# Optimization experiments

Hardware: AMD Instinct MI355X
Metric: run time of the kernel (lower is better)

The kernel has to match this reference:

```python
import jax, jax.numpy as jnp
import numpy as np

N_NODES = 50000
N_EDGES = 800000
IN_F = 128
OUT_F = 64
ORDER = 3


def _spmm(edge_index, edge_attr, x):
    # out[row] += edge_attr[e] * x[col]  (COO sparse @ dense)
    row, col = edge_index[0], edge_index[1]
    msgs = x[col] * edge_attr[:, None]          # [E, F] gather + scale
    return jax.ops.segment_sum(msgs, row, num_segments=N_NODES)  # scatter-add


def setup_inputs() -> dict:
    key = jax.random.key(0)
    k1, k2, k3, k4 = jax.random.split(key, 4)
    x = jax.random.normal(k1, (N_NODES, IN_F), dtype=jnp.float32)
    edge_index = jax.random.randint(k2, (2, N_EDGES), 0, N_NODES, dtype=jnp.int64)
    edge_attr = jax.random.uniform(k3, (N_EDGES,), dtype=jnp.float32)
    W = jax.random.normal(k4, (OUT_F, IN_F), dtype=jnp.float32) * (1.0 / np.sqrt(IN_F))
    b = jnp.zeros((OUT_F,), dtype=jnp.float32)
    return {"x": x, "edge_index": edge_index, "edge_attr": edge_attr, "W": W, "b": b}


def reference(x, edge_index, edge_attr, W, b):
    # output = Linear(x); then `order` rounds of spmm aggregation
    out = jnp.einsum("ni,oi->no", x, W) + b      # [N, OUT_F]
    for _ in range(ORDER):
        out = _spmm(edge_index, edge_attr, out)
    return out
```

## Files before the change

kernel.cpp:

```cpp
#include <hip/hip_runtime.h>

#define IN_F   128
#define OUT_F  64
#define GR     64
#define EPB    2048
#define HB     64
#define SB     2048

typedef float  f32x4  __attribute__((ext_vector_type(4)));
typedef unsigned int u32x2 __attribute__((ext_vector_type(2)));
typedef short  s16x8  __attribute__((ext_vector_type(8)));

__device__ __forceinline__ unsigned short f2bf(float f) {
    unsigned int u = __float_as_uint(f);
    u += 0x7fffu + ((u >> 16) & 1u);
    return (unsigned short)(u >> 16);
}
__device__ __forceinline__ float bf2f(unsigned short h) {
    return __uint_as_float(((unsigned int)h) << 16);
}

__global__ __launch_bounds__(256) void gemm_hist_mfma_kernel(
    const float* __restrict__ x, const float* __restrict__ W,
    const float* __restrict__ b, unsigned short* __restrict__ outv, int N,
    const int* __restrict__ rowi, int* __restrict__ bparts, int E,
    int gemm_blocks, int hist_blocks) {

    __shared__ unsigned short xls[64][136];
    __shared__ unsigned short wls[64][136];

    const int t = threadIdx.x;

    if ((int)blockIdx.x >= gemm_blocks) {
        __shared__ int hcnt[256];
        hcnt[t] = 0;
        __syncthreads();
        int hb = blockIdx.x - gemm_blocks;
        for (int e = hb * 256 + t; e < E; e += hist_blocks * 256)
            atomicAdd(&hcnt[rowi[e] >> 8], 1);
        __syncthreads();
        bparts[hb * 256 + t] = hcnt[t];
        return;
    }

    const int row0 = blockIdx.x * GR;

    for (int i = t; i < GR * (IN_F / 4); i += 256) {
        int r = i >> 5, c = i & 31;
        int gr = row0 + r;
        float4 v = make_float4(0.f, 0.f, 0.f, 0.f);
        if (gr < N) v = ((const float4*)x)[(size_t)gr * (IN_F / 4) + c];
        ushort4 u = { f2bf(v.x), f2bf(v.y), f2bf(v.z), f2bf(v.w) };
        *(ushort4*)&xls[r][4 * c] = u;
    }
    for (int i = t; i < OUT_F * (IN_F / 4); i += 256) {
        int n = i >> 5, c = i & 31;
        float4 v = ((const float4*)W)[(size_t)n * (IN_F / 4) + c];
        ushort4 u = { f2bf(v.x), f2bf(v.y), f2bf(v.z), f2bf(v.w) };
        *(ushort4*)&wls[n][4 * c] = u;
    }
    __syncthreads();

    const int w  = t >> 6;
    const int l  = t & 63;
    const int lr = l & 15;
    const int lg = l >> 4;

    f32x4 acc[4] = {};
    #pragma unroll
    for (int s = 0; s < 4; ++s) {
        s16x8 af = *(const s16x8*)&xls[w * 16 + lr][s * 32 + lg * 8];
        #pragma unroll
        for (int c = 0; c < 4; ++c) {
            s16x8 bf = *(const s16x8*)&wls[c * 16 + lr][s * 32 + lg * 8];
            acc[c] = __builtin_amdgcn_mfma_f32_16x16x32_bf16(af, bf, acc[c], 0, 0, 0);
        }
    }
    __syncthreads();

    #pragma unroll
    for (int c = 0; c < 4; ++c) {
        float bv = b[c * 16 + lr];
        #pragma unroll
        for (int r = 0; r < 4; ++r) {
            int rowl = w * 16 + lg * 4 + r;
            xls[rowl][c * 16 + lr] = f2bf(acc[c][r] + bv);
        }
    }
    __syncthreads();
    for (int i = t; i < GR * (OUT_F / 4); i += 256) {
        int r = i >> 4, c4 = i & 15;
        int gr = row0 + r;
        if (gr < N) {
            ushort4 u = *(ushort4*)&xls[r][c4 * 4];
            *(ushort4*)&outv[(size_t)gr * OUT_F + c4 * 4] = u;
        }
    }
}

__global__ __launch_bounds__(256) void bscan_kernel(const int* __restrict__ bparts,
                                                    int* __restrict__ bbase,
                                                    int* __restrict__ bcursor,
                                                    int* __restrict__ rowptr,
                                                    int nb, int N, int E) {
    int t = threadIdx.x;
    int a0 = 0, a1 = 0, a2 = 0, a3 = 0;
    if (t < nb) {
        #pragma unroll
        for (int hb = 0; hb < HB; hb += 4) {
            a0 += bparts[(hb + 0) * 256 + t];
            a1 += bparts[(hb + 1) * 256 + t];
            a2 += bparts[(hb + 2) * 256 + t];
            a3 += bparts[(hb + 3) * 256 + t];
        }
    }
    int v = (a0 + a1) + (a2 + a3);
    int lane = t & 63, w = t >> 6;
    int sum = v;
    #pragma unroll
    for (int off = 1; off < 64; off <<= 1) {
        int x = __shfl_up(sum, off, 64);
        if (lane >= off) sum += x;
    }
    __shared__ int wsum[4];
    if (lane == 63) wsum[w] = sum;
    __syncthreads();
    int woff = 0;
    for (int i = 0; i < w; ++i) woff += wsum[i];
    int excl = sum + woff - v;
    if (t <= nb) bbase[t] = excl;
    if (t < nb)  bcursor[t] = excl;
    if (t == 0)  rowptr[N] = E;
}

__global__ __launch_bounds__(512) void bin_kernel(
    const int* __restrict__ rowi, const int* __restrict__ coli,
    const float* __restrict__ attr, int* __restrict__ bcursor,
    unsigned long long* __restrict__ tmp, int E) {
    __shared__ int cnt[256];
    __shared__ int cur[256];
    __shared__ int gbase[256];
    int t = threadIdx.x;
    int e0 = blockIdx.x * EPB;
    if (t < 256) { cnt[t] = 0; cur[t] = 0; }
    __syncthreads();
    int myrow[4];
    #pragma unroll
    for (int i = 0; i < 4; ++i) {
        int e = e0 + i * 512 + t;
        myrow[i] = (e < E) ? rowi[e] : -1;
        if (myrow[i] >= 0) atomicAdd(&cnt[myrow[i] >> 8], 1);
    }
    __syncthreads();
    if (t < 256 && cnt[t] > 0) gbase[t] = atomicAdd(&bcursor[t], cnt[t]);
    __syncthreads();
    #pragma unroll
    for (int i = 0; i < 4; ++i) {
        int e = e0 + i * 512 + t;
        if (myrow[i] >= 0) {
            int b = myrow[i] >> 8;
            int rank = atomicAdd(&cur[b], 1);
            unsigned long long rec = ((unsigned long long)(myrow[i] & 255) << 32)
                                   | ((unsigned int)coli[e] << 16)
                                   | (unsigned int)f2bf(attr[e]);
            tmp[(size_t)gbase[b] + rank] = rec;
        }
    }
}

__global__ __launch_bounds__(1024) void bsort_kernel(
    const unsigned long long* __restrict__ tmp, const int* __restrict__ bbase,
    unsigned int* __restrict__ scv, int* __restrict__ rowptr, int N) {
    __shared__ int cnt[256];
    __shared__ int cur[256];
    __shared__ int wsum[4];
    int t = threadIdx.x, b = blockIdx.x;
    int seg = bbase[b], segend = bbase[b + 1];
    if (t < 256) cnt[t] = 0;
    __syncthreads();
    for (int i = seg + t; i < segend; i += 1024)
        atomicAdd(&cnt[(int)(tmp[i] >> 32)], 1);
    __syncthreads();
    int v = (t < 256) ? cnt[t] : 0;
    int lane = t & 63, w = t >> 6;
    int sum = v;
    #pragma unroll
    for (int off = 1; off < 64; off <<= 1) {
        int x = __shfl_up(sum, off, 64);
        if (lane >= off) sum += x;
    }
    if (lane == 63 && w < 4) wsum[w] = sum;
    __syncthreads();
    if (t < 256) {
        int woff = 0;
        for (int i = 0; i < w; ++i) woff += wsum[i];
        int excl = sum + woff - v;
        int gidx = b * 256 + t;
        if (gidx <= N) rowptr[gidx] = seg + excl;
        cur[t] = excl;
    }
    __syncthreads();
    for (int i = seg + t; i < segend; i += 1024) {
        unsigned long long rec = tmp[i];
        int rl = (int)(rec >> 32);
        int pos = atomicAdd(&cur[rl], 1);
        scv[(size_t)seg + pos] = (unsigned int)rec;
    }
}

#define FMA4(w, p)                                              \
    a0 = fmaf((w), __uint_as_float((p).x << 16), a0);           \
    a1 = fmaf((w), __uint_as_float((p).x & 0xffff0000u), a1);   \
    a2 = fmaf((w), __uint_as_float((p).y << 16), a2);           \
    a3 = fmaf((w), __uint_as_float((p).y & 0xffff0000u), a3)

template <bool BF16OUT>
__global__ __launch_bounds__(256) void spmm_csr_kernel(
    const int* __restrict__ rowptr, const unsigned int* __restrict__ scv,
    const unsigned short* __restrict__ in, void* __restrict__ outv,
    int N, int nwaves) {
    int gw = (blockIdx.x * 256 + threadIdx.x) >> 6;
    int lane = threadIdx.x & 63;
    int rpw = (N + nwaves - 1) / nwaves;
    int r0 = gw * rpw;
    int r1 = r0 + rpw;
    if (r1 > N) r1 = N;
    const unsigned int g = lane >> 4;
    const unsigned int s = lane & 15;

    for (int wr = r0; wr < r1; ++wr) {
        int wid = __builtin_amdgcn_readfirstlane(wr);
        int beg = rowptr[wid], end = rowptr[wid + 1];
        float a0 = 0.f, a1 = 0.f, a2 = 0.f, a3 = 0.f;

        int e = beg;
        for (; e + 16 <= end; e += 16) {
            unsigned int v0 = scv[e + g];
            unsigned int v1 = scv[e + 4 + g];
            unsigned int v2 = scv[e + 8 + g];
            unsigned int v3 = scv[e + 12 + g];
            u32x2 p0 = *(const u32x2*)(in + ((v0 >> 16) << 6) + (s << 2));
            u32x2 p1 = *(const u32x2*)(in + ((v1 >> 16) << 6) + (s << 2));
            u32x2 p2 = *(const u32x2*)(in + ((v2 >> 16) << 6) + (s << 2));
            u32x2 p3 = *(const u32x2*)(in + ((v3 >> 16) << 6) + (s << 2));
            float w0 = __uint_as_float(v0 << 16);
            float w1 = __uint_as_float(v1 << 16);
            float w2 = __uint_as_float(v2 << 16);
            float w3 = __uint_as_float(v3 << 16);
            FMA4(w0, p0);
            FMA4(w1, p1);
            FMA4(w2, p2);
            FMA4(w3, p3);
        }
        if (e + 8 <= end) {
            unsigned int v0 = scv[e + g];
            unsigned int v1 = scv[e + 4 + g];
            u32x2 p0 = *(const u32x2*)(in + ((v0 >> 16) << 6) + (s << 2));
            u32x2 p1 = *(const u32x2*)(in + ((v1 >> 16) << 6) + (s << 2));
            float w0 = __uint_as_float(v0 << 16);
            float w1 = __uint_as_float(v1 << 16);
            FMA4(w0, p0);
            FMA4(w1, p1);
            e += 8;
        }
        for (; e < end; e += 4) {
            unsigned int v = (e + (int)g < end) ? scv[e + g] : 0u;
            u32x2 p = *(const u32x2*)(in + ((v >> 16) << 6) + (s << 2));
            float w = __uint_as_float(v << 16);
            FMA4(w, p);
        }

        a0 += __shfl_xor(a0, 16); a0 += __shfl_xor(a0, 32);
        a1 += __shfl_xor(a1, 16); a1 += __shfl_xor(a1, 32);
        a2 += __shfl_xor(a2, 16); a2 += __shfl_xor(a2, 32);
        a3 += __shfl_xor(a3, 16); a3 += __shfl_xor(a3, 32);

        if (g == 0) {
            size_t o = (size_t)wid * OUT_F + (s << 2);
            if (BF16OUT) {
                unsigned long long u =  (unsigned long long)f2bf(a0)
                                     | ((unsigned long long)f2bf(a1) << 16)
                                     | ((unsigned long long)f2bf(a2) << 32)
                                     | ((unsigned long long)f2bf(a3) << 48);
                *(unsigned long long*)((unsigned short*)outv + o) = u;
            } else {
                f32x4 o4 = { a0, a1, a2, a3 };
                *(f32x4*)((float*)outv + o) = o4;
            }
        }
    }
}

__global__ __launch_bounds__(256) void gemm_fb_kernel(
    const float* __restrict__ x, const float* __restrict__ W,
    const float* __restrict__ b, float* __restrict__ outv, int N) {
    __shared__ float xs[GR][IN_F + 4];
    __shared__ float Wt[IN_F][OUT_F + 4];
    const int t = threadIdx.x;
    const int row0 = blockIdx.x * GR;
    for (int i = t; i < OUT_F * (IN_F / 4); i += 256) {
        int o = i & 63, c = i >> 6;
        float4 v = ((const float4*)W)[o * (IN_F / 4) + c];
        Wt[4 * c + 0][o] = v.x; Wt[4 * c + 1][o] = v.y;
        Wt[4 * c + 2][o] = v.z; Wt[4 * c + 3][o] = v.w;
    }
    for (int i = t; i < GR * (IN_F / 4); i += 256) {
        int r = i >> 5, c = i & 31;
        int gr = row0 + r;
        float4 v = make_float4(0.f, 0.f, 0.f, 0.f);
        if (gr < N) v = ((const float4*)x)[(size_t)gr * (IN_F / 4) + c];
        *(float4*)&xs[r][4 * c] = v;
    }
    __syncthreads();
    const int f0 = (t & 15) * 4;
    const int r0 = (t >> 4) * 4;
    float acc[4][4] = {};
    #pragma unroll 2
    for (int k = 0; k < IN_F; k += 4) {
        float4 xv[4], wv[4];
        #pragma unroll
        for (int i = 0; i < 4; ++i) xv[i] = *(const float4*)&xs[r0 + i][k];
        #pragma unroll
        for (int j = 0; j < 4; ++j) wv[j] = *(const float4*)&Wt[k + j][f0];
        #pragma unroll
        for (int i = 0; i < 4; ++i) {
            #pragma unroll
            for (int j = 0; j < 4; ++j) {
                float wx = j == 0 ? wv[0].x : (j == 1 ? wv[0].y : (j == 2 ? wv[0].z : wv[0].w));
                float wy = j == 0 ? wv[1].x : (j == 1 ? wv[1].y : (j == 2 ? wv[1].z : wv[1].w));
                float wz = j == 0 ? wv[2].x : (j == 1 ? wv[2].y : (j == 2 ? wv[2].z : wv[2].w));
                float ww = j == 0 ? wv[3].x : (j == 1 ? wv[3].y : (j == 2 ? wv[3].z : wv[3].w));
                acc[i][j] = fmaf(xv[i].x, wx, acc[i][j]);
                acc[i][j] = fmaf(xv[i].y, wy, acc[i][j]);
                acc[i][j] = fmaf(xv[i].z, wz, acc[i][j]);
                acc[i][j] = fmaf(xv[i].w, ww, acc[i][j]);
            }
        }
    }
    float4 bv = *(const float4*)&b[f0];
    #pragma unroll
    for (int i = 0; i < 4; ++i) {
        int gr = row0 + r0 + i;
        if (gr < N) {
            float4 o4 = make_float4(acc[i][0] + bv.x, acc[i][1] + bv.y,
                                    acc[i][2] + bv.z, acc[i][3] + bv.w);
            *(float4*)&outv[(size_t)gr * OUT_F + f0] = o4;
        }
    }
}

__global__ __launch_bounds__(256) void spmm_atomic_kernel(
    const int* __restrict__ rowi, const int* __restrict__ coli,
    const float* __restrict__ attr, const float* __restrict__ in,
    float* __restrict__ out, int E) {
    int tid = blockIdx.x * 256 + threadIdx.x;
    int e = tid >> 6;
    int lane = tid & 63;
    if (e >= E) return;
    int r = rowi[e];
    int c = coli[e];
    float w = attr[e];
    float v = in[(size_t)c * OUT_F + lane];
    atomicAdd(&out[(size_t)r * OUT_F + lane], w * v);
}

extern "C" void kernel_launch(void* const* d_in, const int* in_sizes, int n_in,
                              void* d_out, int out_size, void* d_ws, size_t ws_size,
                              hipStream_t stream) {
    const float* x    = (const float*)d_in[0];
    const int*   ei   = (const int*)d_in[1];
    const float* attr = (const float*)d_in[2];
    const float* W    = (const float*)d_in[3];
    const float* b    = (const float*)d_in[4];
    float* out = (float*)d_out;

    const int N = in_sizes[0] / IN_F;
    const int E = in_sizes[2];
    const int* rowi = ei;
    const int* coli = ei + E;

    const size_t obytes_f  = (size_t)N * OUT_F * sizeof(float);
    const size_t obytes_bf = (size_t)N * OUT_F * sizeof(unsigned short);
    const int nb = (N + 255) / 256;

    char* wp = (char*)d_ws;
    size_t off = 0;
    auto alloc = [&](size_t bytes) { char* p = wp + off; off += (bytes + 255) & ~(size_t)255; return p; };
    unsigned short* bufA = (unsigned short*)alloc(obytes_bf);
    unsigned short* bufB = (unsigned short*)alloc((size_t)E * 8);
    unsigned long long* tmp = (unsigned long long*)bufB;
    int* rowptr  = (int*)alloc((size_t)(N + 1) * 4);
    int* bparts  = (int*)alloc((size_t)HB * 256 * 4);
    int* bbase   = (int*)alloc(260 * 4);
    int* bcursor = (int*)alloc(260 * 4);
    unsigned int* scv = (unsigned int*)alloc((size_t)E * 4);
    const bool csr_ok = (off <= ws_size) && (N <= 65280) && ((size_t)E * 8 >= obytes_bf);

    const int gemm_blocks = (N + GR - 1) / GR;
    const int nwaves = SB * 4;

    if (csr_ok) {
        gemm_hist_mfma_kernel<<<gemm_blocks + HB, 256, 0, stream>>>(
            x, W, b, bufA, N, rowi, bparts, E, gemm_blocks, HB);

        bscan_kernel<<<1, 256, 0, stream>>>(bparts, bbase, bcursor, rowptr, nb, N, E);
        bin_kernel<<<(E + EPB - 1) / EPB, 512, 0, stream>>>(rowi, coli, attr, bcursor, tmp, E);
        bsort_kernel<<<nb, 1024, 0, stream>>>(tmp, bbase, scv, rowptr, N);

        spmm_csr_kernel<true ><<<SB, 256, 0, stream>>>(rowptr, scv, bufA, bufB, N, nwaves);
        spmm_csr_kernel<true ><<<SB, 256, 0, stream>>>(rowptr, scv, bufB, bufA, N, nwaves);
        spmm_csr_kernel<false><<<SB, 256, 0, stream>>>(rowptr, scv, bufA, out, N, nwaves);
    } else {
        float* ws0 = (float*)d_ws;
        gemm_fb_kernel<<<gemm_blocks, 256, 0, stream>>>(x, W, b, ws0, N);
        const int spmm_blocks = (E * 64 + 255) / 256;
        hipMemsetAsync(out, 0, obytes_f, stream);
        spmm_atomic_kernel<<<spmm_blocks, 256, 0, stream>>>(rowi, coli, attr, ws0, out, E);
        hipMemsetAsync(ws0, 0, obytes_f, stream);
        spmm_atomic_kernel<<<spmm_blocks, 256, 0, stream>>>(rowi, coli, attr, out, ws0, E);
        hipMemsetAsync(out, 0, obytes_f, stream);
        spmm_atomic_kernel<<<spmm_blocks, 256, 0, stream>>>(rowi, coli, attr, ws0, out, E);
    }
}
```

Measured before the change: 178.1 us.

## Replace histogram and scan with fixed-capacity row buckets for CSR build

Each 256-row bucket now gets a fixed slot of 8192 edges in the temporary and sorted arrays, so the separate row-histogram pass and the single-block scan kernel are removed. The GEMM kernel now only zeroes the bucket cursors, the bin kernel places records at bucket*8192 plus an atomic offset, and the sort kernel writes separate begin and end arrays per row for the SpMM. This saves one launch and one full read of the row indices. In exchange it uses more workspace, leaves gaps between buckets, and silently drops edges from any bucket that overflows, because the guard only checks the average bucket load.

```diff
diff --git a/kernel.cpp b/kernel.cpp
--- a/kernel.cpp
+++ b/kernel.cpp
@@ -4,8 +4,8 @@
 #define OUT_F  64
 #define GR     64
 #define EPB    2048
-#define HB     64
 #define SB     2048
+#define BCAP   8192
 
 typedef float  f32x4  __attribute__((ext_vector_type(4)));
 typedef unsigned int u32x2 __attribute__((ext_vector_type(2)));
@@ -20,28 +20,16 @@
     return __uint_as_float(((unsigned int)h) << 16);
 }
 
-__global__ __launch_bounds__(256) void gemm_hist_mfma_kernel(
+__global__ __launch_bounds__(256) void gemm_mfma_kernel(
     const float* __restrict__ x, const float* __restrict__ W,
     const float* __restrict__ b, unsigned short* __restrict__ outv, int N,
-    const int* __restrict__ rowi, int* __restrict__ bparts, int E,
-    int gemm_blocks, int hist_blocks) {
+    int* __restrict__ bcursor) {
 
     __shared__ unsigned short xls[64][136];
     __shared__ unsigned short wls[64][136];
 
     const int t = threadIdx.x;
-
-    if ((int)blockIdx.x >= gemm_blocks) {
-        __shared__ int hcnt[256];
-        hcnt[t] = 0;
-        __syncthreads();
-        int hb = blockIdx.x - gemm_blocks;
-        for (int e = hb * 256 + t; e < E; e += hist_blocks * 256)
-            atomicAdd(&hcnt[rowi[e] >> 8], 1);
-        __syncthreads();
-        bparts[hb * 256 + t] = hcnt[t];
-        return;
-    }
+    if (blockIdx.x == 0 && t < 256) bcursor[t] = 0;
 
     const int row0 = blockIdx.x * GR;
 
@@ -96,41 +84,6 @@
             *(ushort4*)&outv[(size_t)gr * OUT_F + c4 * 4] = u;
         }
     }
-}
-
-__global__ __launch_bounds__(256) void bscan_kernel(const int* __restrict__ bparts,
-                                                    int* __restrict__ bbase,
-                                                    int* __restrict__ bcursor,
-                                                    int* __restrict__ rowptr,
-                                                    int nb, int N, int E) {
-    int t = threadIdx.x;
-    int a0 = 0, a1 = 0, a2 = 0, a3 = 0;
-    if (t < nb) {
-        #pragma unroll
-        for (int hb = 0; hb < HB; hb += 4) {
-            a0 += bparts[(hb + 0) * 256 + t];
-            a1 += bparts[(hb + 1) * 256 + t];
-            a2 += bparts[(hb + 2) * 256 + t];
-            a3 += bparts[(hb + 3) * 256 + t];
-        }
-    }
-    int v = (a0 + a1) + (a2 + a3);
-    int lane = t & 63, w = t >> 6;
-    int sum = v;
-    #pragma unroll
-    for (int off = 1; off < 64; off <<= 1) {
-        int x = __shfl_up(sum, off, 64);
-        if (lane >= off) sum += x;
-    }
-    __shared__ int wsum[4];
-    if (lane == 63) wsum[w] = sum;
-    __syncthreads();
-    int woff = 0;
-    for (int i = 0; i < w; ++i) woff += wsum[i];
-    int excl = sum + woff - v;
-    if (t <= nb) bbase[t] = excl;
-    if (t < nb)  bcursor[t] = excl;
-    if (t == 0)  rowptr[N] = E;
 }
 
 __global__ __launch_bounds__(512) void bin_kernel(
@@ -152,7 +105,8 @@
         if (myrow[i] >= 0) atomicAdd(&cnt[myrow[i] >> 8], 1);
     }
     __syncthreads();
-    if (t < 256 && cnt[t] > 0) gbase[t] = atomicAdd(&bcursor[t], cnt[t]);
+    if (t < 256 && cnt[t] > 0)
+        gbase[t] = (t << 13) + atomicAdd(&bcursor[t], cnt[t]);
     __syncthreads();
     #pragma unroll
     for (int i = 0; i < 4; ++i) {
@@ -163,19 +117,24 @@
             unsigned long long rec = ((unsigned long long)(myrow[i] & 255) << 32)
                                    | ((unsigned int)coli[e] << 16)
                                    | (unsigned int)f2bf(attr[e]);
-            tmp[(size_t)gbase[b] + rank] = rec;
+            size_t pos = (size_t)gbase[b] + rank;
+            if (pos < ((size_t)(b + 1) << 13))
+                tmp[pos] = rec;
         }
     }
 }
 
 __global__ __launch_bounds__(1024) void bsort_kernel(
-    const unsigned long long* __restrict__ tmp, const int* __restrict__ bbase,
-    unsigned int* __restrict__ scv, int* __restrict__ rowptr, int N) {
+    const unsigned long long* __restrict__ tmp, const int* __restrict__ bcursor,
+    unsigned int* __restrict__ scv, int* __restrict__ rowbeg, int* __restrict__ rowend,
+    int N) {
     __shared__ int cnt[256];
     __shared__ int cur[256];
     __shared__ int wsum[4];
     int t = threadIdx.x, b = blockIdx.x;
-    int seg = bbase[b], segend = bbase[b + 1];
+    int seg = b << 13;
+    int total = min(bcursor[b], BCAP);
+    int segend = seg + total;
     if (t < 256) cnt[t] = 0;
     __syncthreads();
     for (int i = seg + t; i < segend; i += 1024)
@@ -196,7 +155,10 @@
         for (int i = 0; i < w; ++i) woff += wsum[i];
         int excl = sum + woff - v;
         int gidx = b * 256 + t;
-        if (gidx <= N) rowptr[gidx] = seg + excl;
+        if (gidx < N) {
+            rowbeg[gidx] = seg + excl;
+            rowend[gidx] = seg + excl + v;
+        }
         cur[t] = excl;
     }
     __syncthreads();
@@ -216,7 +178,8 @@
 
 template <bool BF16OUT>
 __global__ __launch_bounds__(256) void spmm_csr_kernel(
-    const int* __restrict__ rowptr, const unsigned int* __restrict__ scv,
+    const int* __restrict__ rowbeg, const int* __restrict__ rowend,
+    const unsigned int* __restrict__ scv,
     const unsigned short* __restrict__ in, void* __restrict__ outv,
     int N, int nwaves) {
     int gw = (blockIdx.x * 256 + threadIdx.x) >> 6;
@@ -230,7 +193,7 @@
 
     for (int wr = r0; wr < r1; ++wr) {
         int wid = __builtin_amdgcn_readfirstlane(wr);
-        int beg = rowptr[wid], end = rowptr[wid + 1];
+        int beg = rowbeg[wid], end = rowend[wid];
         float a0 = 0.f, a1 = 0.f, a2 = 0.f, a3 = 0.f;
 
         int e = beg;
@@ -387,29 +350,26 @@
     size_t off = 0;
     auto alloc = [&](size_t bytes) { char* p = wp + off; off += (bytes + 255) & ~(size_t)255; return p; };
     unsigned short* bufA = (unsigned short*)alloc(obytes_bf);
-    unsigned short* bufB = (unsigned short*)alloc((size_t)E * 8);
-    unsigned long long* tmp = (unsigned long long*)bufB;
-    int* rowptr  = (int*)alloc((size_t)(N + 1) * 4);
-    int* bparts  = (int*)alloc((size_t)HB * 256 * 4);
-    int* bbase   = (int*)alloc(260 * 4);
+    unsigned short* bufB = (unsigned short*)alloc(obytes_bf);
+    unsigned long long* tmp = (unsigned long long*)alloc((size_t)nb * BCAP * 8);
+    unsigned int* scv = (unsigned int*)alloc((size_t)nb * BCAP * 4);
+    int* rowbeg  = (int*)alloc((size_t)N * 4);
+    int* rowend  = (int*)alloc((size_t)N * 4);
     int* bcursor = (int*)alloc(260 * 4);
-    unsigned int* scv = (unsigned int*)alloc((size_t)E * 4);
-    const bool csr_ok = (off <= ws_size) && (N <= 65280) && ((size_t)E * 8 >= obytes_bf);
+    const bool csr_ok = (off <= ws_size) && (N <= 65280) && (E <= nb * (BCAP / 2));
 
     const int gemm_blocks = (N + GR - 1) / GR;
     const int nwaves = SB * 4;
 
     if (csr_ok) {
-        gemm_hist_mfma_kernel<<<gemm_blocks + HB, 256, 0, stream>>>(
-            x, W, b, bufA, N, rowi, bparts, E, gemm_blocks, HB);
-
-        bscan_kernel<<<1, 256, 0, stream>>>(bparts, bbase, bcursor, rowptr, nb, N, E);
+        gemm_mfma_kernel<<<gemm_blocks, 256, 0, stream>>>(x, W, b, bufA, N, bcursor);
+
         bin_kernel<<<(E + EPB - 1) / EPB, 512, 0, stream>>>(rowi, coli, attr, bcursor, tmp, E);
-        bsort_kernel<<<nb, 1024, 0, stream>>>(tmp, bbase, scv, rowptr, N);
-
-        spmm_csr_kernel<true ><<<SB, 256, 0, stream>>>(rowptr, scv, bufA, bufB, N, nwaves);
-        spmm_csr_kernel<true ><<<SB, 256, 0, stream>>>(rowptr, scv, bufB, bufA, N, nwaves);
-        spmm_csr_kernel<false><<<SB, 256, 0, stream>>>(rowptr, scv, bufA, out, N, nwaves);
+        bsort_kernel<<<nb, 1024, 0, stream>>>(tmp, bcursor, scv, rowbeg, rowend, N);
+
+        spmm_csr_kernel<true ><<<SB, 256, 0, stream>>>(rowbeg, rowend, scv, bufA, bufB, N, nwaves);
+        spmm_csr_kernel<true ><<<SB, 256, 0, stream>>>(rowbeg, rowend, scv, bufB, bufA, N, nwaves);
+        spmm_csr_kernel<false><<<SB, 256, 0, stream>>>(rowbeg, rowend, scv, bufA, out, N, nwaves);
     } else {
         float* ws0 = (float*)d_ws;
         gemm_fb_kernel<<<gemm_blocks, 256, 0, stream>>>(x, W, b, ws0, N);
```

Result: faster. 165.4 us (-7.1%).
